# Optimization experiments

Hardware: AMD Instinct MI355X
Metric: run time of the kernel (lower is better)

The kernel has to match this reference:

```python
import jax, jax.numpy as jnp
import numpy as np

N = 50000      # nodes
E = 800000     # edges (avg degree 16)
F_IN = 128     # input features
HID = 64       # hidden per head
HEADS = 4      # heads per layer
G = 256        # graphs in batch
C = 10         # classes
ALPHA = 0.01   # leaky relu negative slope


def setup_inputs() -> dict:
    key = jax.random.key(0)
    ks = jax.random.split(key, 12)
    x = jax.random.normal(ks[0], (N, F_IN), dtype=jnp.float32)
    edge_index = jax.random.randint(ks[1], (2, E), 0, N, dtype=jnp.int32)
    batch = jnp.sort(jax.random.randint(ks[2], (N,), 0, G, dtype=jnp.int32))

    def glorot(k, shape):
        fan_in = shape[0] if len(shape) == 2 else int(np.prod(shape[1:]))
        return (jax.random.normal(k, shape, dtype=jnp.float32) / np.float32(np.sqrt(fan_in)))

    W1 = glorot(ks[3], (F_IN, HEADS * HID))
    a1_src = glorot(ks[4], (HEADS, HID))
    a1_dst = glorot(ks[5], (HEADS, HID))
    W2 = glorot(ks[6], (HEADS * HID, HEADS * HID))
    a2_src = glorot(ks[7], (HEADS, HID))
    a2_dst = glorot(ks[8], (HEADS, HID))
    lin_W = glorot(ks[9], (2 * HEADS * HID, C))
    lin_b = jnp.zeros((C,), dtype=jnp.float32)
    return {
        "x": x, "edge_index": edge_index, "batch": batch,
        "W1": W1, "a1_src": a1_src, "a1_dst": a1_dst,
        "W2": W2, "a2_src": a2_src, "a2_dst": a2_dst,
        "lin_W": lin_W, "lin_b": lin_b,
    }


def _gat_layer(x, src, dst, W, a_src, a_dst):
    """Multi-head GAT layer: edge softmax over incoming neighbors, concat heads, ELU."""
    n = x.shape[0]
    h, f = a_src.shape
    Wh = (x @ W).reshape(n, h, f)                       # [N,H,F]
    # per-node attention logits (decomposed GAT attention a^T [Wh_i || Wh_j])
    ls = jnp.einsum("nhf,hf->nh", Wh, a_src)            # [N,H]
    ld = jnp.einsum("nhf,hf->nh", Wh, a_dst)            # [N,H]
    e = jax.nn.leaky_relu(ls[src] + ld[dst], ALPHA)      # [E,H]
    # numerically-stable softmax over edges grouped by destination node
    m = jax.ops.segment_max(e, dst, num_segments=n)      # [N,H]
    m = jnp.where(jnp.isfinite(m), m, 0.0)
    p = jnp.exp(e - m[dst])                              # [E,H]
    z = jax.ops.segment_sum(p, dst, num_segments=n)      # [N,H]
    attn = p / (z[dst] + 1e-16)                          # [E,H]
    msg = Wh[src] * attn[:, :, None]                     # [E,H,F]
    out = jax.ops.segment_sum(msg, dst, num_segments=n)  # [N,H,F]
    return jax.nn.elu(out.reshape(n, h * f))


def reference(x, edge_index, batch, W1, a1_src, a1_dst, W2, a2_src, a2_dst, lin_W, lin_b):
    src, dst = edge_index[0], edge_index[1]
    x = _gat_layer(x, src, dst, W1, a1_src, a1_dst)
    x = _gat_layer(x, src, dst, W2, a2_src, a2_dst)
    # global max / mean pool per graph
    mx = jax.ops.segment_max(x, batch, num_segments=G)
    mx = jnp.where(jnp.isfinite(mx), mx, 0.0)
    s = jax.ops.segment_sum(x, batch, num_segments=G)
    cnt = jax.ops.segment_sum(jnp.ones((x.shape[0], 1), x.dtype), batch, num_segments=G)
    mean = s / jnp.maximum(cnt, 1.0)
    pooled = jnp.concatenate([mx, mean], axis=1)         # [G, 2*H*F]
    return pooled @ lin_W + lin_b                        # [G, C]
```

## Files before the change

### kernel.cpp

```cpp
#include <hip/hip_runtime.h>
#include <hip/hip_bf16.h>

#define NNODES 50000
#define NEDGES 800000
#define FIN    128
#define HID    64
#define HEADS  4
#define NGRAPH 256
#define NCLS   10
#define DTOT   256
#define ALPHA  0.01f
#define CAPLG  6
#define CAP    (1 << CAPLG)

typedef short bf16x8 __attribute__((ext_vector_type(8)));
typedef float f32x4  __attribute__((ext_vector_type(4)));

#define NB      ((NNODES + 255) / 256)
#define EB      ((NEDGES + 255) / 256)
#define W1B     (FIN * DTOT / 256)
#define W2B     (DTOT * DTOT / 256)

__device__ __forceinline__ ushort f2bf(float v) {
    return __bfloat16_as_ushort(__float2bfloat16(v));
}
__device__ __forceinline__ float blo(unsigned u) { return __uint_as_float(u << 16); }
__device__ __forceinline__ float bhi(unsigned u) { return __uint_as_float(u & 0xffff0000u); }
__device__ __forceinline__ unsigned pack2(float lo, float hi) {
    return ((unsigned)f2bf(hi) << 16) | (unsigned)f2bf(lo);
}
__device__ __forceinline__ bf16x8 cvt8(float4 lo, float4 hi) {
    bf16x8 r;
    r[0] = (short)f2bf(lo.x); r[1] = (short)f2bf(lo.y);
    r[2] = (short)f2bf(lo.z); r[3] = (short)f2bf(lo.w);
    r[4] = (short)f2bf(hi.x); r[5] = (short)f2bf(hi.y);
    r[6] = (short)f2bf(hi.z); r[7] = (short)f2bf(hi.w);
    return r;
}

__global__ __launch_bounds__(256) void k_setup(const int* __restrict__ src, const int* __restrict__ dst,
                                               int* __restrict__ cursor, ushort* __restrict__ esrc,
                                               const int* __restrict__ batch, int* __restrict__ gstart,
                                               const float* __restrict__ W1, ushort* __restrict__ W1t,
                                               const float* __restrict__ W2, ushort* __restrict__ W2t) {
    int b = blockIdx.x, t = threadIdx.x;
    if (b < EB) {
        int e = b * 256 + t;
        if (e < NEDGES) {
            int d = dst[e];
            int pos = atomicAdd(&cursor[d], 1);
            if (pos < CAP) esrc[(d << CAPLG) + pos] = (ushort)src[e];
        }
    } else if (b < EB + NB) {
        int i = (b - EB) * 256 + t;
        if (i >= NNODES) return;
        int bb = batch[i];
        if (i == 0) {
            for (int g = 0; g <= bb; ++g) gstart[g] = 0;
        } else {
            int pb = batch[i - 1];
            if (pb != bb) for (int g = pb + 1; g <= bb; ++g) gstart[g] = i;
        }
        if (i == NNODES - 1)
            for (int g = bb + 1; g <= NGRAPH; ++g) gstart[g] = NNODES;
    } else if (b < EB + NB + W1B) {
        int id = (b - EB - NB) * 256 + t;
        int n = id & 255, k = id >> 8;
        W1t[n * FIN + (((k >> 3) ^ (n & 7)) << 3) + (k & 7)] = f2bf(W1[k * DTOT + n]);
    } else {
        int id = (b - EB - NB - W1B) * 256 + t;
        int n = id & 255, k = id >> 8;
        W2t[n * DTOT + (((k >> 3) ^ (n & 7)) << 3) + (k & 7)] = f2bf(W2[k * DTOT + n]);
    }
}

template <int K, bool AF32>
__global__ __launch_bounds__(512, 4) void k_gemm_mfma(const void* __restrict__ Aptr,
                                                      const ushort* __restrict__ Bt,
                                                      ushort* __restrict__ Cbf,
                                                      float* __restrict__ ls,
                                                      float* __restrict__ ld_,
                                                      const float* __restrict__ a_src,
                                                      const float* __restrict__ a_dst,
                                                      int M) {
    constexpr int NC = K / 64;
    __shared__ ushort Bl[2][256 * 64];
    const int tid  = threadIdx.x;
    const int w    = tid >> 6;
    const int lane = tid & 63;
    const int l15  = lane & 15;
    const int quad = lane >> 4;
    const int m0 = blockIdx.x * 128;

    f32x4 acc[16];
#pragma unroll
    for (int nf = 0; nf < 16; ++nf) acc[nf] = (f32x4){0.f, 0.f, 0.f, 0.f};

    int rowA0 = m0 + w * 16 + l15;  if (rowA0 >= M) rowA0 = M - 1;
    const ushort* pa0b = (const ushort*)Aptr + (size_t)rowA0 * K + quad * 8;
    const float*  pa0f = (const float*)Aptr  + (size_t)rowA0 * K + quad * 8;

    uint4 rg[4];
#pragma unroll
    for (int it = 0; it < 4; ++it) {
        int idx = tid + it * 512;
        int n = idx >> 3, c8 = (idx ^ n) & 7;
        rg[it] = *(const uint4*)&Bt[(size_t)n * K + c8 * 8];
    }
#pragma unroll
    for (int it = 0; it < 4; ++it) {
        int idx = tid + it * 512;
        int n = idx >> 3, c8 = (idx ^ n) & 7;
        *(uint4*)&Bl[0][n * 64 + c8 * 8] = rg[it];
    }
    __syncthreads();

#pragma unroll
    for (int kc = 0; kc < NC; ++kc) {
        if (kc + 1 < NC) {
#pragma unroll
            for (int it = 0; it < 4; ++it) {
                int idx = tid + it * 512;
                int n = idx >> 3, c8 = (idx ^ n) & 7;
                rg[it] = *(const uint4*)&Bt[(size_t)n * K + (kc + 1) * 64 + c8 * 8];
            }
        }
#pragma unroll
        for (int ks = 0; ks < 2; ++ks) {
            bf16x8 a0;
            if constexpr (AF32) {
                const float* p = pa0f + kc * 64 + ks * 32;
                float4 alo = *(const float4*)p;
                float4 ahi = *(const float4*)(p + 4);
                a0 = cvt8(alo, ahi);
            } else {
                a0 = *(const bf16x8*)(pa0b + kc * 64 + ks * 32);
            }
#pragma unroll
            for (int nh = 0; nh < 4; ++nh) {
                bf16x8 bfr[4];
#pragma unroll
                for (int j = 0; j < 4; ++j) {
                    int n = (nh * 4 + j) * 16 + l15;
                    int c = (ks * 4 + quad) ^ (n & 7);
                    bfr[j] = *(const bf16x8*)&Bl[kc & 1][n * 64 + (c << 3)];
                }
#pragma unroll
                for (int j = 0; j < 4; ++j)
                    acc[nh * 4 + j] = __builtin_amdgcn_mfma_f32_16x16x32_bf16(a0, bfr[j], acc[nh * 4 + j], 0, 0, 0);
            }
        }
        if (kc + 1 < NC) {
#pragma unroll
            for (int it = 0; it < 4; ++it) {
                int idx = tid + it * 512;
                int n = idx >> 3, c8 = (idx ^ n) & 7;
                *(uint4*)&Bl[(kc + 1) & 1][n * 64 + c8 * 8] = rg[it];
            }
        }
        __syncthreads();
    }

    float as[16], ad[16];
#pragma unroll
    for (int nf = 0; nf < 16; ++nf) {
        int head = nf >> 2;
        as[nf] = a_src[head * HID + (nf & 3) * 16 + l15];
        ad[nf] = a_dst[head * HID + (nf & 3) * 16 + l15];
    }
#pragma unroll
    for (int reg = 0; reg < 4; ++reg) {
        int row = m0 + w * 16 + quad * 4 + reg;
        bool ok = row < M;
        if (ok) {
#pragma unroll
            for (int nf = 0; nf < 16; ++nf)
                Cbf[(size_t)row * DTOT + nf * 16 + l15] = f2bf(acc[nf][reg]);
        }
        float sh[4], dh[4];
#pragma unroll
        for (int head = 0; head < 4; ++head) {
            float s = 0.f, d = 0.f;
#pragma unroll
            for (int j = 0; j < 4; ++j) {
                int nf = head * 4 + j;
                s += acc[nf][reg] * as[nf];
                d += acc[nf][reg] * ad[nf];
            }
            sh[head] = s; dh[head] = d;
        }
#pragma unroll
        for (int off = 1; off < 16; off <<= 1) {
#pragma unroll
            for (int head = 0; head < 4; ++head) {
                sh[head] += __shfl_xor(sh[head], off);
                dh[head] += __shfl_xor(dh[head], off);
            }
        }
        if (ok && l15 == 0) {
#pragma unroll
            for (int head = 0; head < 4; ++head) {
                ls[row * HEADS + head]  = sh[head];
                ld_[row * HEADS + head] = dh[head];
            }
        }
    }
}

__global__ __launch_bounds__(256) void k_gat_aggr(const int* __restrict__ cnt,
                                                  const ushort* __restrict__ esrc,
                                                  const ushort* __restrict__ Whbf,
                                                  const float* __restrict__ ls,
                                                  const float* __restrict__ ld_,
                                                  ushort* __restrict__ out) {
    const int wv   = threadIdx.x >> 6;
    const int lane = threadIdx.x & 63;
    const int i    = blockIdx.x * 4 + wv;
    if (i >= NNODES) return;
    const int half = lane >> 5;
    const int l32  = lane & 31;
    const int h    = l32 >> 3;
    const int e0 = i << CAPLG;
    int deg = cnt[i]; if (deg > CAP) deg = CAP;
    const int e1 = e0 + deg;
    const float ldv = ld_[i * HEADS + h];

    float ac[8] = {};
    float z = 0.f;
    const int ch = 8 * l32;
    int e = e0 + half;
    for (; e + 6 < e1; e += 8) {
        int s0 = (int)esrc[e], s1 = (int)esrc[e + 2], s2 = (int)esrc[e + 4], s3 = (int)esrc[e + 6];
        float l0 = ls[s0 * HEADS + h] + ldv;
        float l1 = ls[s1 * HEADS + h] + ldv;
        float l2 = ls[s2 * HEADS + h] + ldv;
        float l3 = ls[s3 * HEADS + h] + ldv;
        uint4 u0 = *(const uint4*)&Whbf[(size_t)s0 * DTOT + ch];
        uint4 u1 = *(const uint4*)&Whbf[(size_t)s1 * DTOT + ch];
        uint4 u2 = *(const uint4*)&Whbf[(size_t)s2 * DTOT + ch];
        uint4 u3 = *(const uint4*)&Whbf[(size_t)s3 * DTOT + ch];
        float p0 = __expf(l0 > 0.f ? l0 : ALPHA * l0);
        float p1 = __expf(l1 > 0.f ? l1 : ALPHA * l1);
        float p2 = __expf(l2 > 0.f ? l2 : ALPHA * l2);
        float p3 = __expf(l3 > 0.f ? l3 : ALPHA * l3);
        z += p0 + p1 + p2 + p3;
        ac[0] = fmaf(p0, blo(u0.x), ac[0]); ac[1] = fmaf(p0, bhi(u0.x), ac[1]);
        ac[2] = fmaf(p0, blo(u0.y), ac[2]); ac[3] = fmaf(p0, bhi(u0.y), ac[3]);
        ac[4] = fmaf(p0, blo(u0.z), ac[4]); ac[5] = fmaf(p0, bhi(u0.z), ac[5]);
        ac[6] = fmaf(p0, blo(u0.w), ac[6]); ac[7] = fmaf(p0, bhi(u0.w), ac[7]);
        ac[0] = fmaf(p1, blo(u1.x), ac[0]); ac[1] = fmaf(p1, bhi(u1.x), ac[1]);
        ac[2] = fmaf(p1, blo(u1.y), ac[2]); ac[3] = fmaf(p1, bhi(u1.y), ac[3]);
        ac[4] = fmaf(p1, blo(u1.z), ac[4]); ac[5] = fmaf(p1, bhi(u1.z), ac[5]);
        ac[6] = fmaf(p1, blo(u1.w), ac[6]); ac[7] = fmaf(p1, bhi(u1.w), ac[7]);
        ac[0] = fmaf(p2, blo(u2.x), ac[0]); ac[1] = fmaf(p2, bhi(u2.x), ac[1]);
        ac[2] = fmaf(p2, blo(u2.y), ac[2]); ac[3] = fmaf(p2, bhi(u2.y), ac[3]);
        ac[4] = fmaf(p2, blo(u2.z), ac[4]); ac[5] = fmaf(p2, bhi(u2.z), ac[5]);
        ac[6] = fmaf(p2, blo(u2.w), ac[6]); ac[7] = fmaf(p2, bhi(u2.w), ac[7]);
        ac[0] = fmaf(p3, blo(u3.x), ac[0]); ac[1] = fmaf(p3, bhi(u3.x), ac[1]);
        ac[2] = fmaf(p3, blo(u3.y), ac[2]); ac[3] = fmaf(p3, bhi(u3.y), ac[3]);
        ac[4] = fmaf(p3, blo(u3.z), ac[4]); ac[5] = fmaf(p3, bhi(u3.z), ac[5]);
        ac[6] = fmaf(p3, blo(u3.w), ac[6]); ac[7] = fmaf(p3, bhi(u3.w), ac[7]);
    }
    for (; e < e1; e += 2) {
        int s0 = (int)esrc[e];
        float l0 = ls[s0 * HEADS + h] + ldv;
        uint4 u0 = *(const uint4*)&Whbf[(size_t)s0 * DTOT + ch];
        float p0 = __expf(l0 > 0.f ? l0 : ALPHA * l0);
        z += p0;
        ac[0] = fmaf(p0, blo(u0.x), ac[0]); ac[1] = fmaf(p0, bhi(u0.x), ac[1]);
        ac[2] = fmaf(p0, blo(u0.y), ac[2]); ac[3] = fmaf(p0, bhi(u0.y), ac[3]);
        ac[4] = fmaf(p0, blo(u0.z), ac[4]); ac[5] = fmaf(p0, bhi(u0.z), ac[5]);
        ac[6] = fmaf(p0, blo(u0.w), ac[6]); ac[7] = fmaf(p0, bhi(u0.w), ac[7]);
    }

#pragma unroll
    for (int j = 0; j < 8; ++j) ac[j] += __shfl_xor(ac[j], 32);
    z += __shfl_xor(z, 32);

    if (half == 0) {
        const float inv = 1.f / (z + 1e-16f);
        float v[8];
#pragma unroll
        for (int j = 0; j < 8; ++j) {
            float t = ac[j] * inv;
            v[j] = t > 0.f ? t : __expf(t) - 1.f;
        }
        uint4 pk;
        pk.x = pack2(v[0], v[1]);
        pk.y = pack2(v[2], v[3]);
        pk.z = pack2(v[4], v[5]);
        pk.w = pack2(v[6], v[7]);
        *(uint4*)(out + (size_t)i * DTOT + ch) = pk;
    }
}

__global__ __launch_bounds__(1024) void k_pool_final(const ushort* __restrict__ h2bf,
                                                     const int* __restrict__ gstart,
                                                     const float* __restrict__ W,
                                                     const float* __restrict__ b,
                                                     float* __restrict__ out) {
    __shared__ float smx[16][256];
    __shared__ float ssm[16][256];
    __shared__ float pooled[2 * DTOT];
    int g = blockIdx.x, t = threadIdx.x;
    int cg = t & 31, j = t >> 5;
    int s = gstart[g], e = gstart[g + 1];
    float mx[8], sm[8];
#pragma unroll
    for (int k = 0; k < 8; ++k) { mx[k] = -INFINITY; sm[k] = 0.f; }
    for (int n = s + j; n < e; n += 32) {
        uint4 u = *(const uint4*)&h2bf[(size_t)n * DTOT + cg * 8];
        float v0 = blo(u.x), v1 = bhi(u.x), v2 = blo(u.y), v3 = bhi(u.y);
        float v4 = blo(u.z), v5 = bhi(u.z), v6 = blo(u.w), v7 = bhi(u.w);
        mx[0] = fmaxf(mx[0], v0); sm[0] += v0;
        mx[1] = fmaxf(mx[1], v1); sm[1] += v1;
        mx[2] = fmaxf(mx[2], v2); sm[2] += v2;
        mx[3] = fmaxf(mx[3], v3); sm[3] += v3;
        mx[4] = fmaxf(mx[4], v4); sm[4] += v4;
        mx[5] = fmaxf(mx[5], v5); sm[5] += v5;
        mx[6] = fmaxf(mx[6], v6); sm[6] += v6;
        mx[7] = fmaxf(mx[7], v7); sm[7] += v7;
    }
#pragma unroll
    for (int k = 0; k < 8; ++k) {
        mx[k] = fmaxf(mx[k], __shfl_xor(mx[k], 32));
        sm[k] += __shfl_xor(sm[k], 32);
    }
    int wave = t >> 6, lane = t & 63;
    if (lane < 32) {
        *(float4*)&smx[wave][lane * 8]     = make_float4(mx[0], mx[1], mx[2], mx[3]);
        *(float4*)&smx[wave][lane * 8 + 4] = make_float4(mx[4], mx[5], mx[6], mx[7]);
        *(float4*)&ssm[wave][lane * 8]     = make_float4(sm[0], sm[1], sm[2], sm[3]);
        *(float4*)&ssm[wave][lane * 8 + 4] = make_float4(sm[4], sm[5], sm[6], sm[7]);
    }
    __syncthreads();
    if (t < 256) {
        float m = -INFINITY, su = 0.f;
#pragma unroll
        for (int jj = 0; jj < 16; ++jj) {
            m = fmaxf(m, smx[jj][t]);
            su += ssm[jj][t];
        }
        int cnt = e - s;
        if (cnt <= 0) m = 0.f;
        pooled[t] = m;
        pooled[DTOT + t] = su / (float)(cnt > 0 ? cnt : 1);
    }
    __syncthreads();
    int wv = t >> 6;
    if (wv < NCLS) {
        float acc = 0.f;
        for (int k = lane; k < 2 * DTOT; k += 64)
            acc += pooled[k] * W[k * NCLS + wv];
#pragma unroll
        for (int off = 32; off; off >>= 1) acc += __shfl_down(acc, off);
        if (lane == 0)
            out[g * NCLS + wv] = acc + b[wv];
    }
}

extern "C" void kernel_launch(void* const* d_in, const int* in_sizes, int n_in,
                              void* d_out, int out_size, void* d_ws, size_t ws_size,
                              hipStream_t stream) {
    const float* x     = (const float*)d_in[0];
    const int*   ei    = (const int*)d_in[1];
    const int*   batch = (const int*)d_in[2];
    const float* W1    = (const float*)d_in[3];
    const float* a1s   = (const float*)d_in[4];
    const float* a1d   = (const float*)d_in[5];
    const float* W2    = (const float*)d_in[6];
    const float* a2s   = (const float*)d_in[7];
    const float* a2d   = (const float*)d_in[8];
    const float* linW  = (const float*)d_in[9];
    const float* linb  = (const float*)d_in[10];
    float* out = (float*)d_out;

    const int* src = ei;
    const int* dst = ei + NEDGES;

    size_t off = 0;
    char* base = (char*)d_ws;
    auto alloc = [&](size_t bytes) -> void* {
        void* p = base + off;
        off += (bytes + 255) & ~(size_t)255;
        return p;
    };
    ushort* Whbf   = (ushort*)alloc((size_t)NNODES * DTOT * 2);
    ushort* h1bf   = (ushort*)alloc((size_t)NNODES * DTOT * 2);
    ushort* h2bf   = (ushort*)alloc((size_t)NNODES * DTOT * 2);
    float*  ls     = (float*)alloc((size_t)NNODES * HEADS * 4);
    float*  ld_    = (float*)alloc((size_t)NNODES * HEADS * 4);
    int*    cursor = (int*)alloc((size_t)NNODES * 4);
    ushort* esrc   = (ushort*)alloc((size_t)(NNODES << CAPLG) * 2);
    int*    gstart = (int*)alloc((size_t)(NGRAPH + 1) * 4);
    ushort* W1t    = (ushort*)alloc((size_t)DTOT * FIN * 2);
    ushort* W2t    = (ushort*)alloc((size_t)DTOT * DTOT * 2);

    hipMemsetAsync(cursor, 0, (size_t)NNODES * 4, stream);

    int setup_blocks = EB + NB + W1B + W2B;
    k_setup<<<setup_blocks, 256, 0, stream>>>(src, dst, cursor, esrc, batch, gstart,
                                              W1, W1t, W2, W2t);

    int ggrid = (NNODES + 127) / 128;

    k_gemm_mfma<FIN, true><<<ggrid, 512, 0, stream>>>((const void*)x, W1t, Whbf, ls, ld_, a1s, a1d, NNODES);
    k_gat_aggr<<<(NNODES + 3) / 4, 256, 0, stream>>>(cursor, esrc, Whbf, ls, ld_, h1bf);

    k_gemm_mfma<DTOT, false><<<ggrid, 512, 0, stream>>>((const void*)h1bf, W2t, Whbf, ls, ld_, a2s, a2d, NNODES);
    k_gat_aggr<<<(NNODES + 3) / 4, 256, 0, stream>>>(cursor, esrc, Whbf, ls, ld_, h2bf);

    k_pool_final<<<NGRAPH, 1024, 0, stream>>>(h2bf, gstart, linW, linb, out);
}
```

Measured before the change: 321.3 us.

## Replace double-buffered LDS B staging with single-buffer load-sync-compute loop

The GEMM kernel drops the double-buffered shared-memory tile of B and its register prefetch. Each K chunk is now loaded straight into one LDS buffer, synchronised, and then consumed, and the minimum-blocks launch hint is removed. This halves LDS use and lowers register pressure, which could raise occupancy, but global-load latency is no longer overlapped with the MFMA work.

```diff
diff --git a/kernel.cpp b/kernel.cpp
--- a/kernel.cpp
+++ b/kernel.cpp
@@ -75,16 +75,15 @@
 }
 
 template <int K, bool AF32>
-__global__ __launch_bounds__(512, 4) void k_gemm_mfma(const void* __restrict__ Aptr,
-                                                      const ushort* __restrict__ Bt,
-                                                      ushort* __restrict__ Cbf,
-                                                      float* __restrict__ ls,
-                                                      float* __restrict__ ld_,
-                                                      const float* __restrict__ a_src,
-                                                      const float* __restrict__ a_dst,
-                                                      int M) {
-    constexpr int NC = K / 64;
-    __shared__ ushort Bl[2][256 * 64];
+__global__ __launch_bounds__(512) void k_gemm_mfma(const void* __restrict__ Aptr,
+                                                   const ushort* __restrict__ Bt,
+                                                   ushort* __restrict__ Cbf,
+                                                   float* __restrict__ ls,
+                                                   float* __restrict__ ld_,
+                                                   const float* __restrict__ a_src,
+                                                   const float* __restrict__ a_dst,
+                                                   int M) {
+    __shared__ ushort Bl[256 * 64];
     const int tid  = threadIdx.x;
     const int w    = tid >> 6;
     const int lane = tid & 63;
@@ -100,31 +99,17 @@
     const ushort* pa0b = (const ushort*)Aptr + (size_t)rowA0 * K + quad * 8;
     const float*  pa0f = (const float*)Aptr  + (size_t)rowA0 * K + quad * 8;
 
-    uint4 rg[4];
-#pragma unroll
-    for (int it = 0; it < 4; ++it) {
-        int idx = tid + it * 512;
-        int n = idx >> 3, c8 = (idx ^ n) & 7;
-        rg[it] = *(const uint4*)&Bt[(size_t)n * K + c8 * 8];
-    }
-#pragma unroll
-    for (int it = 0; it < 4; ++it) {
-        int idx = tid + it * 512;
-        int n = idx >> 3, c8 = (idx ^ n) & 7;
-        *(uint4*)&Bl[0][n * 64 + c8 * 8] = rg[it];
-    }
-    __syncthreads();
-
-#pragma unroll
-    for (int kc = 0; kc < NC; ++kc) {
-        if (kc + 1 < NC) {
-#pragma unroll
-            for (int it = 0; it < 4; ++it) {
-                int idx = tid + it * 512;
+#pragma unroll
+    for (int kc = 0; kc < K / 64; ++kc) {
+        {
+#pragma unroll
+            for (int idx = tid; idx < 2048; idx += 512) {
                 int n = idx >> 3, c8 = (idx ^ n) & 7;
-                rg[it] = *(const uint4*)&Bt[(size_t)n * K + (kc + 1) * 64 + c8 * 8];
-            }
-        }
+                *(uint4*)&Bl[n * 64 + c8 * 8] =
+                    *(const uint4*)&Bt[(size_t)n * K + kc * 64 + c8 * 8];
+            }
+        }
+        __syncthreads();
 #pragma unroll
         for (int ks = 0; ks < 2; ++ks) {
             bf16x8 a0;
@@ -143,19 +128,11 @@
                 for (int j = 0; j < 4; ++j) {
                     int n = (nh * 4 + j) * 16 + l15;
                     int c = (ks * 4 + quad) ^ (n & 7);
-                    bfr[j] = *(const bf16x8*)&Bl[kc & 1][n * 64 + (c << 3)];
+                    bfr[j] = *(const bf16x8*)&Bl[n * 64 + (c << 3)];
                 }
 #pragma unroll
                 for (int j = 0; j < 4; ++j)
                     acc[nh * 4 + j] = __builtin_amdgcn_mfma_f32_16x16x32_bf16(a0, bfr[j], acc[nh * 4 + j], 0, 0, 0);
-            }
-        }
-        if (kc + 1 < NC) {
-#pragma unroll
-            for (int it = 0; it < 4; ++it) {
-                int idx = tid + it * 512;
-                int n = idx >> 3, c8 = (idx ^ n) & 7;
-                *(uint4*)&Bl[(kc + 1) & 1][n * 64 + c8 * 8] = rg[it];
             }
         }
         __syncthreads();
```

New measurement: 306.4 us. 1.05x faster.
